# Kernel tuning notes

Measured on AMD Instinct MI355X. Metric: run time of the kernel, lower is better.

The kernel has to match this reference:

```python
import jax, jax.numpy as jnp
import numpy as np

B, NT, NZ, CIN, H, DOUT, L = 16, 128, 256, 3, 64, 128, 3
N = NT * NZ  # 32768 nodes
EPS = 1e-5


def _build_edges():
    # Toroidal grid: each node connects to 4 neighbors (wrap-around in theta and zeta).
    T, Z = np.meshgrid(np.arange(NT), np.arange(NZ), indexing='ij')
    curr = (T * NZ + Z).ravel()
    nbrs = np.stack([
        (((T + 1) % NT) * NZ + Z).ravel(),
        (((T - 1) % NT) * NZ + Z).ravel(),
        (T * NZ + (Z + 1) % NZ).ravel(),
        (T * NZ + (Z - 1) % NZ).ravel(),
    ], axis=1)
    src = np.repeat(curr, 4)
    dst = nbrs.ravel()
    return np.stack([src, dst]).astype(np.int32)  # (2, 4N)


def setup_inputs() -> dict:
    key = jax.random.key(0)
    ks = jax.random.split(key, 8)
    s = lambda k, shp, fan: jax.random.normal(k, shp, jnp.float32) / np.float32(np.sqrt(fan))
    return {
        'x': jax.random.normal(ks[0], (B, CIN, N), jnp.float32),
        'edge_index': jnp.asarray(_build_edges()),
        'embed_W': s(ks[1], (CIN, H), CIN),
        'embed_b': jnp.zeros((H,), jnp.float32),
        'mp_W1': s(ks[2], (L, 2 * H, H), 2 * H),
        'mp_b1': jnp.zeros((L, H), jnp.float32),
        'mp_g1': jnp.ones((L, H), jnp.float32),
        'mp_be1': jnp.zeros((L, H), jnp.float32),
        'mp_W2': s(ks[3], (L, H, H), H),
        'mp_b2': jnp.zeros((L, H), jnp.float32),
        'mp_g2': jnp.ones((L, H), jnp.float32),
        'mp_be2': jnp.zeros((L, H), jnp.float32),
        'head_W1': s(ks[4], (H, H), H),
        'head_b1': jnp.zeros((H,), jnp.float32),
        'head_W2': s(ks[5], (H, DOUT), H),
        'head_b2': jnp.zeros((DOUT,), jnp.float32),
    }


def _bn(y, g, b):
    # BatchNorm1d in training mode: biased batch stats over (batch*nodes).
    m = y.mean(axis=(0, 1))
    v = y.var(axis=(0, 1))
    return (y - m) * (g * jax.lax.rsqrt(v + EPS)) + b


def reference(x, edge_index, embed_W, embed_b, mp_W1, mp_b1, mp_g1, mp_be1,
              mp_W2, mp_b2, mp_g2, mp_be2, head_W1, head_b1, head_W2, head_b2):
    src, dst = edge_index[0], edge_index[1]
    # embedding: (B,3,N) -> (B,N,H)
    h = jax.nn.relu(jnp.einsum('bcn,ch->bnh', x, embed_W) + embed_b)
    deg = jnp.zeros((N,), x.dtype).at[dst].add(1.0)
    deg = jnp.clip(deg, 1.0)[None, :, None]  # (1,N,1), all 4 on this graph
    for l in range(L):
        # gather neighbor features and scatter-add to destination, mean aggregate
        agg = jnp.zeros_like(h).at[:, dst, :].add(h[:, src, :]) / deg
        comb = jnp.concatenate([h, agg], axis=-1)  # (B,N,2H)
        y = jax.nn.relu(_bn(comb @ mp_W1[l] + mp_b1[l], mp_g1[l], mp_be1[l]))
        y = jax.nn.relu(_bn(y @ mp_W2[l] + mp_b2[l], mp_g2[l], mp_be2[l]))
        h = y + h  # residual (c_in == c_out)
    pooled = h.mean(axis=1)  # AdaptiveAvgPool1d(1) over nodes
    return jax.nn.relu(pooled @ head_W1 + head_b1) @ head_W2 + head_b2
```

## Files before the change

kernel.cpp:

```cpp
#include <hip/hip_runtime.h>

typedef unsigned short u16;
typedef u16 u16x8 __attribute__((ext_vector_type(8)));
typedef short s16x8 __attribute__((ext_vector_type(8)));
typedef float f32x4 __attribute__((ext_vector_type(4)));

#define NNODES 32768
#define EPSV 1e-5f
#define INV_ROWS (1.0f / 524288.0f)

__device__ __forceinline__ float bf2f(u16 u) {
  union { unsigned int i; float f; } v; v.i = ((unsigned int)u) << 16; return v.f;
}
__device__ __forceinline__ u16 f2bf(float f) {
  union { float f; unsigned int i; } v; v.f = f;
  unsigned int r = v.i + 0x7FFFu + ((v.i >> 16) & 1u);
  return (u16)(r >> 16);
}

__global__ __launch_bounds__(256) void k_prep(
    const float* __restrict__ W1, const float* __restrict__ W2,
    u16* __restrict__ w1t, u16* __restrict__ w2t) {
  int idx = blockIdx.x * 256 + threadIdx.x;
  if (idx < 24576) {
    int l = idx >> 13, rem = idx & 8191;
    int n = rem >> 7, k = rem & 127;
    float w = W1[l * 8192 + k * 64 + n];
    if (k >= 64) w *= 0.25f;
    w1t[idx] = f2bf(w);
  } else {
    int idx2 = idx - 24576;
    if (idx2 < 12288) {
      int l = idx2 >> 12, rem = idx2 & 4095;
      int n = rem >> 6, k = rem & 63;
      w2t[idx2] = f2bf(W2[l * 4096 + k * 64 + n]);
    }
  }
}

__global__ __launch_bounds__(256) void k_embed(
    const float* __restrict__ x, const float* __restrict__ eW,
    const float* __restrict__ eb, u16* __restrict__ h) {
  int tid = threadIdx.x;
  int chunk = tid & 7;
  int r = blockIdx.x * 32 + (tid >> 3);
  int b = r >> 15;
  int n = r & 32767;
  const float* xb = x + (size_t)b * 3 * NNODES + n;
  float x0 = xb[0], x1 = xb[NNODES], x2 = xb[2 * NNODES];
  int c0 = chunk * 8;
  u16x8 ov;
#pragma unroll
  for (int j = 0; j < 8; ++j) {
    float acc = eb[c0 + j] + x0 * eW[c0 + j] + x1 * eW[64 + c0 + j] + x2 * eW[128 + c0 + j];
    ov[j] = f2bf(fmaxf(acc, 0.f));
  }
  *reinterpret_cast<u16x8*>(&h[(size_t)r * 64 + c0]) = ov;
}

#define RSTR 72
__global__ __launch_bounds__(256) void k_gemm1(
    const u16* __restrict__ h, u16* __restrict__ ybuf,
    const u16* __restrict__ w1t, const float* __restrict__ b1,
    float* __restrict__ sums) {
  __shared__ __align__(16) u16 buf[2][194 * RSTR];
  __shared__ __align__(16) u16 t_s[4][16 * RSTR];
  __shared__ float stat_s[4][128];

  int tid = threadIdx.x;
  int wv = tid >> 6, ln = tid & 63, ln15 = ln & 15, quad = ln >> 4;
  int blk = blockIdx.x;
  int xcd = blk & 7;
  int j = blk >> 3;
  int b = j >> 4;
  int t = xcd * 16 + (j & 15);
  const u16* hb = h + (((size_t)b) << 15) * 64;
  int tp = (t + 1) & 127, tm = (t + 127) & 127;

  s16x8 bfT[4][2], bfB[4][2];
#pragma unroll
  for (int c = 0; c < 4; ++c)
#pragma unroll
    for (int kk = 0; kk < 2; ++kk) {
      bfT[c][kk] = *reinterpret_cast<const s16x8*>(
          &w1t[(c * 16 + ln15) * 128 + kk * 32 + quad * 8]);
      bfB[c][kk] = *reinterpret_cast<const s16x8*>(
          &w1t[(c * 16 + ln15) * 128 + 64 + kk * 32 + quad * 8]);
    }

  float bias_c[4];
#pragma unroll
  for (int c = 0; c < 4; ++c) bias_c[c] = b1[c * 16 + ln15];

  float ls[4] = {0.f, 0.f, 0.f, 0.f}, ls2[4] = {0.f, 0.f, 0.f, 0.f};
  u16* ts = &t_s[wv][0];
  int cA = quad * 8;

  u16x8 R[7];
  auto ld_regs = [&](int q) {
    int z0 = q * 64;
#pragma unroll
    for (int ii = 0; ii < 7; ++ii) {
      int i = tid + ii * 256;
      if (i < 1552) {
        int c = i & 7;
        int r, rt, z;
        if (i < 528)       { r = i >> 3;          rt = t;  z = (z0 + 255 + r) & 255; }
        else if (i < 1040) { r = (i - 528) >> 3;  rt = tp; z = z0 + r; }
        else               { r = (i - 1040) >> 3; rt = tm; z = z0 + r; }
        R[ii] = *reinterpret_cast<const u16x8*>(
            &hb[((size_t)(rt * 256 + z)) * 64 + c * 8]);
      }
    }
  };
  auto wr_lds = [&](int bi) {
    u16* B = &buf[bi][0];
#pragma unroll
    for (int ii = 0; ii < 7; ++ii) {
      int i = tid + ii * 256;
      if (i < 1552) {
        int c = i & 7;
        int off;
        if (i < 528)       off = (i >> 3) * RSTR;
        else if (i < 1040) off = (66 + ((i - 528) >> 3)) * RSTR;
        else               off = (130 + ((i - 1040) >> 3)) * RSTR;
        *reinterpret_cast<u16x8*>(&B[off + c * 8]) = R[ii];
      }
    }
  };
  auto compute = [&](int q, int bi) {
    const u16* S  = &buf[bi][0];
    const u16* Tp = &buf[bi][66 * RSTR];
    const u16* Tm = &buf[bi][130 * RSTR];
    int lr = wv * 16 + ln15;

    s16x8 s0  = *reinterpret_cast<const s16x8*>(&S[(lr + 1) * RSTR + cA]);
    s16x8 s1  = *reinterpret_cast<const s16x8*>(&S[(lr + 1) * RSTR + 32 + cA]);
    s16x8 n0a = *reinterpret_cast<const s16x8*>(&Tp[lr * RSTR + cA]);
    s16x8 n0b = *reinterpret_cast<const s16x8*>(&Tp[lr * RSTR + 32 + cA]);
    s16x8 n1a = *reinterpret_cast<const s16x8*>(&Tm[lr * RSTR + cA]);
    s16x8 n1b = *reinterpret_cast<const s16x8*>(&Tm[lr * RSTR + 32 + cA]);
    s16x8 n2a = *reinterpret_cast<const s16x8*>(&S[(lr + 2) * RSTR + cA]);
    s16x8 n2b = *reinterpret_cast<const s16x8*>(&S[(lr + 2) * RSTR + 32 + cA]);
    s16x8 n3a = *reinterpret_cast<const s16x8*>(&S[lr * RSTR + cA]);
    s16x8 n3b = *reinterpret_cast<const s16x8*>(&S[lr * RSTR + 32 + cA]);

    f32x4 acc[4];
#pragma unroll
    for (int c = 0; c < 4; ++c) acc[c] = (f32x4){0.f, 0.f, 0.f, 0.f};
#pragma unroll
    for (int c = 0; c < 4; ++c) {
      acc[c] = __builtin_amdgcn_mfma_f32_16x16x32_bf16(s0,  bfT[c][0], acc[c], 0, 0, 0);
      acc[c] = __builtin_amdgcn_mfma_f32_16x16x32_bf16(s1,  bfT[c][1], acc[c], 0, 0, 0);
      acc[c] = __builtin_amdgcn_mfma_f32_16x16x32_bf16(n0a, bfB[c][0], acc[c], 0, 0, 0);
      acc[c] = __builtin_amdgcn_mfma_f32_16x16x32_bf16(n0b, bfB[c][1], acc[c], 0, 0, 0);
      acc[c] = __builtin_amdgcn_mfma_f32_16x16x32_bf16(n1a, bfB[c][0], acc[c], 0, 0, 0);
      acc[c] = __builtin_amdgcn_mfma_f32_16x16x32_bf16(n1b, bfB[c][1], acc[c], 0, 0, 0);
      acc[c] = __builtin_amdgcn_mfma_f32_16x16x32_bf16(n2a, bfB[c][0], acc[c], 0, 0, 0);
      acc[c] = __builtin_amdgcn_mfma_f32_16x16x32_bf16(n2b, bfB[c][1], acc[c], 0, 0, 0);
      acc[c] = __builtin_amdgcn_mfma_f32_16x16x32_bf16(n3a, bfB[c][0], acc[c], 0, 0, 0);
      acc[c] = __builtin_amdgcn_mfma_f32_16x16x32_bf16(n3b, bfB[c][1], acc[c], 0, 0, 0);
    }

    __builtin_amdgcn_wave_barrier();
#pragma unroll
    for (int c = 0; c < 4; ++c)
#pragma unroll
      for (int rg = 0; rg < 4; ++rg) {
        float vy = acc[c][rg] + bias_c[c];
        ls[c] += vy;
        ls2[c] += vy * vy;
        ts[(quad * 4 + rg) * RSTR + c * 16 + ln15] = f2bf(vy);
      }
    __builtin_amdgcn_wave_barrier();
    size_t R0 = (((size_t)b) << 15) + (size_t)t * 256 + q * 64 + wv * 16;
    int lr2 = ln >> 2;
#pragma unroll
    for (int p = 0; p < 2; ++p) {
      int ck = (ln & 3) + p * 4;
      u16x8 v = *reinterpret_cast<const u16x8*>(&ts[lr2 * RSTR + ck * 8]);
      *reinterpret_cast<u16x8*>(&ybuf[(R0 + lr2) * 64 + ck * 8]) = v;
    }
    __builtin_amdgcn_wave_barrier();
  };

  ld_regs(0);
  wr_lds(0);
  __syncthreads();
#pragma unroll 1
  for (int q = 0; q < 4; ++q) {
    if (q < 3) ld_regs(q + 1);
    compute(q, q & 1);
    if (q < 3) {
      wr_lds((q + 1) & 1);
      __syncthreads();
    }
  }

#pragma unroll
  for (int c = 0; c < 4; ++c) {
    ls[c]  += __shfl_xor(ls[c], 16, 64);  ls[c]  += __shfl_xor(ls[c], 32, 64);
    ls2[c] += __shfl_xor(ls2[c], 16, 64); ls2[c] += __shfl_xor(ls2[c], 32, 64);
  }
  if (ln < 16) {
#pragma unroll
    for (int c = 0; c < 4; ++c) {
      stat_s[wv][c * 16 + ln] = ls[c];
      stat_s[wv][64 + c * 16 + ln] = ls2[c];
    }
  }
  __syncthreads();
  if (tid < 128) {
    float s = stat_s[0][tid] + stat_s[1][tid] + stat_s[2][tid] + stat_s[3][tid];
    atomicAdd(&sums[xcd * 128 + tid], s);
  }
}

__global__ __launch_bounds__(256) void k_gemm2(
    u16* __restrict__ ybuf, const u16* __restrict__ w2t,
    const float* __restrict__ b2, const float* __restrict__ sums1,
    const float* __restrict__ g1, const float* __restrict__ be1,
    float* __restrict__ sums2) {
  __shared__ __align__(16) u16 t_s[4][16 * RSTR];
  __shared__ float s1_s[64], sh1_s[64];
  __shared__ float stat_s[4][128];

  int tid = threadIdx.x;
  int wv = tid >> 6, ln = tid & 63, ln15 = ln & 15, quad = ln >> 4;

  if (tid < 64) {
    float s = 0.f, s2 = 0.f;
#pragma unroll
    for (int sl = 0; sl < 8; ++sl) { s += sums1[sl * 128 + tid]; s2 += sums1[sl * 128 + 64 + tid]; }
    float m = s * INV_ROWS;
    float v = s2 * INV_ROWS - m * m;
    float sc = g1[tid] * rsqrtf(v + EPSV);
    s1_s[tid] = sc;
    sh1_s[tid] = be1[tid] - m * sc;
  }

  s16x8 bf[4][2];
#pragma unroll
  for (int c = 0; c < 4; ++c)
#pragma unroll
    for (int kk = 0; kk < 2; ++kk)
      bf[c][kk] = *reinterpret_cast<const s16x8*>(
          &w2t[(c * 16 + ln15) * 64 + kk * 32 + quad * 8]);

  float bias_c[4];
#pragma unroll
  for (int c = 0; c < 4; ++c) bias_c[c] = b2[c * 16 + ln15];

  __syncthreads();

  float sA[2][8], shA[2][8];
#pragma unroll
  for (int kk = 0; kk < 2; ++kk)
#pragma unroll
    for (int j = 0; j < 8; ++j) {
      int ch = kk * 32 + quad * 8 + j;
      sA[kk][j] = s1_s[ch];
      shA[kk][j] = sh1_s[ch];
    }

  float ls[4] = {0.f, 0.f, 0.f, 0.f}, ls2[4] = {0.f, 0.f, 0.f, 0.f};
  u16* ts = &t_s[wv][0];

  auto ld2 = [&](int it, u16x8* Y) {
    size_t row = (size_t)blockIdx.x * 256 + it * 64 + wv * 16 + ln15;
    Y[0] = *reinterpret_cast<const u16x8*>(&ybuf[row * 64 + quad * 8]);
    Y[1] = *reinterpret_cast<const u16x8*>(&ybuf[row * 64 + 32 + quad * 8]);
  };

  auto consume2 = [&](int it, u16x8* Y) {
    s16x8 a0, a1;
#pragma unroll
    for (int j = 0; j < 8; ++j) {
      a0[j] = (short)f2bf(fmaxf(bf2f(Y[0][j]) * sA[0][j] + shA[0][j], 0.f));
      a1[j] = (short)f2bf(fmaxf(bf2f(Y[1][j]) * sA[1][j] + shA[1][j], 0.f));
    }
    f32x4 acc[4];
#pragma unroll
    for (int c = 0; c < 4; ++c) acc[c] = (f32x4){0.f, 0.f, 0.f, 0.f};
#pragma unroll
    for (int c = 0; c < 4; ++c) {
      acc[c] = __builtin_amdgcn_mfma_f32_16x16x32_bf16(a0, bf[c][0], acc[c], 0, 0, 0);
      acc[c] = __builtin_amdgcn_mfma_f32_16x16x32_bf16(a1, bf[c][1], acc[c], 0, 0, 0);
    }
    __builtin_amdgcn_wave_barrier();
#pragma unroll
    for (int c = 0; c < 4; ++c)
#pragma unroll
      for (int rg = 0; rg < 4; ++rg) {
        float vy = acc[c][rg] + bias_c[c];
        ls[c] += vy;
        ls2[c] += vy * vy;
        ts[(quad * 4 + rg) * RSTR + c * 16 + ln15] = f2bf(vy);
      }
    __builtin_amdgcn_wave_barrier();
    size_t r0 = (size_t)blockIdx.x * 256 + it * 64 + wv * 16;
    int lr = ln >> 2;
#pragma unroll
    for (int p = 0; p < 2; ++p) {
      int ck = (ln & 3) + p * 4;
      u16x8 v = *reinterpret_cast<const u16x8*>(&ts[lr * RSTR + ck * 8]);
      *reinterpret_cast<u16x8*>(&ybuf[(r0 + lr) * 64 + ck * 8]) = v;
    }
    __builtin_amdgcn_wave_barrier();
  };

  u16x8 YA[2], YB[2];
  ld2(0, YA);
#pragma unroll 1
  for (int it = 0; it < 4; it += 2) {
    ld2(it + 1, YB);
    consume2(it, YA);
    if (it + 2 < 4) ld2(it + 2, YA);
    consume2(it + 1, YB);
  }

#pragma unroll
  for (int c = 0; c < 4; ++c) {
    ls[c]  += __shfl_xor(ls[c], 16, 64);  ls[c]  += __shfl_xor(ls[c], 32, 64);
    ls2[c] += __shfl_xor(ls2[c], 16, 64); ls2[c] += __shfl_xor(ls2[c], 32, 64);
  }
  if (ln < 16) {
#pragma unroll
    for (int c = 0; c < 4; ++c) {
      stat_s[wv][c * 16 + ln] = ls[c];
      stat_s[wv][64 + c * 16 + ln] = ls2[c];
    }
  }
  __syncthreads();
  if (tid < 128) {
    float s = stat_s[0][tid] + stat_s[1][tid] + stat_s[2][tid] + stat_s[3][tid];
    atomicAdd(&sums2[(blockIdx.x & 7) * 128 + tid], s);
  }
}

__global__ __launch_bounds__(256) void k_resid(
    u16* __restrict__ h, const u16* __restrict__ zbuf,
    const float* __restrict__ sums2, const float* __restrict__ g2,
    const float* __restrict__ be2, float* __restrict__ pooled) {
  __shared__ float s2_s[64], sh2_s[64];
  __shared__ float red_s[32][68];
  int tid = threadIdx.x;
  if (tid < 64) {
    float s = 0.f, s2 = 0.f;
#pragma unroll
    for (int sl = 0; sl < 8; ++sl) { s += sums2[sl * 128 + tid]; s2 += sums2[sl * 128 + 64 + tid]; }
    float m = s * INV_ROWS;
    float v = s2 * INV_ROWS - m * m;
    float sc = g2[tid] * rsqrtf(v + EPSV);
    s2_s[tid] = sc;
    sh2_s[tid] = be2[tid] - m * sc;
  }
  __syncthreads();
  int ch0 = (tid & 7) * 8;
  float scl[8], shl[8];
#pragma unroll
  for (int j = 0; j < 8; ++j) { scl[j] = s2_s[ch0 + j]; shl[j] = sh2_s[ch0 + j]; }
  float p[8] = {0.f, 0.f, 0.f, 0.f, 0.f, 0.f, 0.f, 0.f};
  bool do_pool = (pooled != nullptr);
  size_t base0 = (size_t)blockIdx.x * 16384 + tid * 8;
#pragma unroll 1
  for (int it = 0; it < 8; it += 2) {
    size_t ba = base0 + it * 2048;
    size_t bb = ba + 2048;
    u16x8 zva = *reinterpret_cast<const u16x8*>(&zbuf[ba]);
    u16x8 hva = *reinterpret_cast<const u16x8*>(&h[ba]);
    u16x8 zvb = *reinterpret_cast<const u16x8*>(&zbuf[bb]);
    u16x8 hvb = *reinterpret_cast<const u16x8*>(&h[bb]);
    u16x8 ova, ovb;
#pragma unroll
    for (int j = 0; j < 8; ++j) {
      float a = fmaxf(bf2f(zva[j]) * scl[j] + shl[j], 0.f);
      ova[j] = f2bf(bf2f(hva[j]) + a);
      p[j] += bf2f(ova[j]);
    }
#pragma unroll
    for (int j = 0; j < 8; ++j) {
      float a = fmaxf(bf2f(zvb[j]) * scl[j] + shl[j], 0.f);
      ovb[j] = f2bf(bf2f(hvb[j]) + a);
      p[j] += bf2f(ovb[j]);
    }
    if (!do_pool) {
      *reinterpret_cast<u16x8*>(&h[ba]) = ova;
      *reinterpret_cast<u16x8*>(&h[bb]) = ovb;
    }
  }
  if (do_pool) {
    int g = tid >> 3;
#pragma unroll
    for (int j = 0; j < 8; ++j) red_s[g][ch0 + j] = p[j];
    __syncthreads();
    if (tid < 64) {
      float s = 0.f;
#pragma unroll
      for (int gg = 0; gg < 32; ++gg) s += red_s[gg][tid];
      atomicAdd(&pooled[(blockIdx.x >> 7) * 64 + tid], s);
    }
  }
}

__global__ __launch_bounds__(256) void k_head(
    const float* __restrict__ pooled, const float* __restrict__ hW1,
    const float* __restrict__ hb1, const float* __restrict__ hW2,
    const float* __restrict__ hb2, float* __restrict__ out) {
  __shared__ float p_s[16 * 64];
  __shared__ float t1_s[16 * 64];
  int tid = threadIdx.x;
#pragma unroll
  for (int j = 0; j < 4; ++j)
    p_s[tid + 256 * j] = pooled[tid + 256 * j] * (1.0f / 32768.0f);
  __syncthreads();
#pragma unroll
  for (int j = 0; j < 4; ++j) {
    int idx = tid + 256 * j;
    int bb = idx >> 6, o = idx & 63;
    float acc = hb1[o];
    for (int k = 0; k < 64; ++k) acc += p_s[bb * 64 + k] * hW1[k * 64 + o];
    t1_s[idx] = fmaxf(acc, 0.f);
  }
  __syncthreads();
#pragma unroll
  for (int j = 0; j < 8; ++j) {
    int idx = tid + 256 * j;
    int bb = idx >> 7, o = idx & 127;
    float acc = hb2[o];
    for (int k = 0; k < 64; ++k) acc += t1_s[bb * 64 + k] * hW2[k * 128 + o];
    out[idx] = acc;
  }
}

extern "C" void kernel_launch(void* const* d_in, const int* in_sizes, int n_in,
                              void* d_out, int out_size, void* d_ws, size_t ws_size,
                              hipStream_t stream) {
  const float* x   = (const float*)d_in[0];
  const float* eW  = (const float*)d_in[2];
  const float* eb  = (const float*)d_in[3];
  const float* W1  = (const float*)d_in[4];
  const float* b1  = (const float*)d_in[5];
  const float* g1  = (const float*)d_in[6];
  const float* be1 = (const float*)d_in[7];
  const float* W2  = (const float*)d_in[8];
  const float* b2  = (const float*)d_in[9];
  const float* g2  = (const float*)d_in[10];
  const float* be2 = (const float*)d_in[11];
  const float* hW1 = (const float*)d_in[12];
  const float* hb1 = (const float*)d_in[13];
  const float* hW2 = (const float*)d_in[14];
  const float* hb2 = (const float*)d_in[15];
  float* out = (float*)d_out;

  char* ws = (char*)d_ws;
  u16* h    = (u16*)ws;
  u16* ybuf = (u16*)(ws + 67108864);
  float* stats  = (float*)(ws + 134217728);
  float* pooled = stats + 6144;
  u16* w1t = (u16*)(ws + 134217728 + 7168 * 4);
  u16* w2t = w1t + 24576;

  hipMemsetAsync(stats, 0, (6144 + 1024) * sizeof(float), stream);

  k_prep<<<144, 256, 0, stream>>>(W1, W2, w1t, w2t);
  k_embed<<<16384, 256, 0, stream>>>(x, eW, eb, h);
  for (int l = 0; l < 3; ++l) {
    float* sum1 = stats + l * 2048;
    float* sum2 = stats + l * 2048 + 1024;
    k_gemm1<<<2048, 256, 0, stream>>>(h, ybuf, w1t + l * 8192, b1 + l * 64, sum1);
    k_gemm2<<<2048, 256, 0, stream>>>(ybuf, w2t + l * 4096, b2 + l * 64,
                                      sum1, g1 + l * 64, be1 + l * 64, sum2);
    k_resid<<<2048, 256, 0, stream>>>(h, ybuf, sum2, g2 + l * 64, be2 + l * 64,
                                      (l == 2) ? pooled : nullptr);
  }
  k_head<<<1, 256, 0, stream>>>(pooled, hW1, hb1, hW2, hb2, out);
}
```

Baseline: 414.0 us.

## Process two theta rows per gemm1 block with XOR-swizzled LDS and fuse prep into embed

Each gemm1 block now handles two adjacent theta rows, loading four halo rows (t-1, t0, t1, t+1) so the middle rows are shared and fewer neighbor rows are reloaded from global memory. The grid is halved and each wave computes two 16-row tiles. LDS padding is replaced by an XOR chunk swizzle to avoid bank conflicts with a denser layout, which grows LDS use per block. Weight conversion is folded into the embed kernel, removing one launch.

```diff
diff --git a/kernel.cpp b/kernel.cpp
--- a/kernel.cpp
+++ b/kernel.cpp
@@ -18,29 +18,11 @@
   return (u16)(r >> 16);
 }
 
-__global__ __launch_bounds__(256) void k_prep(
+__global__ __launch_bounds__(256) void k_embed(
+    const float* __restrict__ x, const float* __restrict__ eW,
+    const float* __restrict__ eb, u16* __restrict__ h,
     const float* __restrict__ W1, const float* __restrict__ W2,
     u16* __restrict__ w1t, u16* __restrict__ w2t) {
-  int idx = blockIdx.x * 256 + threadIdx.x;
-  if (idx < 24576) {
-    int l = idx >> 13, rem = idx & 8191;
-    int n = rem >> 7, k = rem & 127;
-    float w = W1[l * 8192 + k * 64 + n];
-    if (k >= 64) w *= 0.25f;
-    w1t[idx] = f2bf(w);
-  } else {
-    int idx2 = idx - 24576;
-    if (idx2 < 12288) {
-      int l = idx2 >> 12, rem = idx2 & 4095;
-      int n = rem >> 6, k = rem & 63;
-      w2t[idx2] = f2bf(W2[l * 4096 + k * 64 + n]);
-    }
-  }
-}
-
-__global__ __launch_bounds__(256) void k_embed(
-    const float* __restrict__ x, const float* __restrict__ eW,
-    const float* __restrict__ eb, u16* __restrict__ h) {
   int tid = threadIdx.x;
   int chunk = tid & 7;
   int r = blockIdx.x * 32 + (tid >> 3);
@@ -56,15 +38,28 @@
     ov[j] = f2bf(fmaxf(acc, 0.f));
   }
   *reinterpret_cast<u16x8*>(&h[(size_t)r * 64 + c0]) = ov;
-}
-
-#define RSTR 72
+
+  int pidx = blockIdx.x * 256 + tid;
+  if (pidx < 24576) {
+    int l = pidx >> 13, rem = pidx & 8191;
+    int nn = rem >> 7, k = rem & 127;
+    float w = W1[l * 8192 + k * 64 + nn];
+    if (k >= 64) w *= 0.25f;
+    w1t[pidx] = f2bf(w);
+  } else if (pidx < 36864) {
+    int idx2 = pidx - 24576;
+    int l = idx2 >> 12, rem = idx2 & 4095;
+    int nn = rem >> 6, k = rem & 63;
+    w2t[idx2] = f2bf(W2[l * 4096 + k * 64 + nn]);
+  }
+}
+
 __global__ __launch_bounds__(256) void k_gemm1(
     const u16* __restrict__ h, u16* __restrict__ ybuf,
     const u16* __restrict__ w1t, const float* __restrict__ b1,
     float* __restrict__ sums) {
-  __shared__ __align__(16) u16 buf[2][194 * RSTR];
-  __shared__ __align__(16) u16 t_s[4][16 * RSTR];
+  __shared__ __align__(16) u16 buf[2][4 * 66 * 64];
+  __shared__ __align__(16) u16 t_s[4][16 * 64];
   __shared__ float stat_s[4][128];
 
   int tid = threadIdx.x;
@@ -72,10 +67,12 @@
   int blk = blockIdx.x;
   int xcd = blk & 7;
   int j = blk >> 3;
-  int b = j >> 4;
-  int t = xcd * 16 + (j & 15);
+  int b = j >> 3;
+  int local = j & 7;
+  int t0 = xcd * 16 + local * 2;
+  int t1 = t0 + 1;
   const u16* hb = h + (((size_t)b) << 15) * 64;
-  int tp = (t + 1) & 127, tm = (t + 127) & 127;
+  int tm = (t0 + 127) & 127, tp3 = (t1 + 1) & 127;
 
   s16x8 bfT[4][2], bfB[4][2];
 #pragma unroll
@@ -93,21 +90,19 @@
   for (int c = 0; c < 4; ++c) bias_c[c] = b1[c * 16 + ln15];
 
   float ls[4] = {0.f, 0.f, 0.f, 0.f}, ls2[4] = {0.f, 0.f, 0.f, 0.f};
-  u16* ts = &t_s[wv][0];
-  int cA = quad * 8;
-
-  u16x8 R[7];
+
+  u16x8 R[9];
   auto ld_regs = [&](int q) {
     int z0 = q * 64;
 #pragma unroll
-    for (int ii = 0; ii < 7; ++ii) {
+    for (int ii = 0; ii < 9; ++ii) {
       int i = tid + ii * 256;
-      if (i < 1552) {
+      if (i < 2112) {
+        int g = (i >= 1056) ? ((i >= 1584) ? 3 : 2) : ((i >= 528) ? 1 : 0);
+        int rr = (i - g * 528) >> 3;
         int c = i & 7;
-        int r, rt, z;
-        if (i < 528)       { r = i >> 3;          rt = t;  z = (z0 + 255 + r) & 255; }
-        else if (i < 1040) { r = (i - 528) >> 3;  rt = tp; z = z0 + r; }
-        else               { r = (i - 1040) >> 3; rt = tm; z = z0 + r; }
+        int rt = (g == 0) ? tm : (g == 1) ? t0 : (g == 2) ? t1 : tp3;
+        int z = (z0 + 255 + rr) & 255;
         R[ii] = *reinterpret_cast<const u16x8*>(
             &hb[((size_t)(rt * 256 + z)) * 64 + c * 8]);
       }
@@ -116,72 +111,85 @@
   auto wr_lds = [&](int bi) {
     u16* B = &buf[bi][0];
 #pragma unroll
-    for (int ii = 0; ii < 7; ++ii) {
+    for (int ii = 0; ii < 9; ++ii) {
       int i = tid + ii * 256;
-      if (i < 1552) {
+      if (i < 2112) {
+        int g = (i >= 1056) ? ((i >= 1584) ? 3 : 2) : ((i >= 528) ? 1 : 0);
+        int rr = (i - g * 528) >> 3;
         int c = i & 7;
-        int off;
-        if (i < 528)       off = (i >> 3) * RSTR;
-        else if (i < 1040) off = (66 + ((i - 528) >> 3)) * RSTR;
-        else               off = (130 + ((i - 1040) >> 3)) * RSTR;
-        *reinterpret_cast<u16x8*>(&B[off + c * 8]) = R[ii];
+        *reinterpret_cast<u16x8*>(
+            &B[(g * 66 + rr) * 64 + ((c ^ (rr & 7)) << 3)]) = R[ii];
       }
     }
   };
+  auto lds_rd = [&](const u16* base, int row, int chunk) {
+    return *reinterpret_cast<const s16x8*>(
+        &base[row * 64 + ((chunk ^ (row & 7)) << 3)]);
+  };
   auto compute = [&](int q, int bi) {
-    const u16* S  = &buf[bi][0];
-    const u16* Tp = &buf[bi][66 * RSTR];
-    const u16* Tm = &buf[bi][130 * RSTR];
-    int lr = wv * 16 + ln15;
-
-    s16x8 s0  = *reinterpret_cast<const s16x8*>(&S[(lr + 1) * RSTR + cA]);
-    s16x8 s1  = *reinterpret_cast<const s16x8*>(&S[(lr + 1) * RSTR + 32 + cA]);
-    s16x8 n0a = *reinterpret_cast<const s16x8*>(&Tp[lr * RSTR + cA]);
-    s16x8 n0b = *reinterpret_cast<const s16x8*>(&Tp[lr * RSTR + 32 + cA]);
-    s16x8 n1a = *reinterpret_cast<const s16x8*>(&Tm[lr * RSTR + cA]);
-    s16x8 n1b = *reinterpret_cast<const s16x8*>(&Tm[lr * RSTR + 32 + cA]);
-    s16x8 n2a = *reinterpret_cast<const s16x8*>(&S[(lr + 2) * RSTR + cA]);
-    s16x8 n2b = *reinterpret_cast<const s16x8*>(&S[(lr + 2) * RSTR + 32 + cA]);
-    s16x8 n3a = *reinterpret_cast<const s16x8*>(&S[lr * RSTR + cA]);
-    s16x8 n3b = *reinterpret_cast<const s16x8*>(&S[lr * RSTR + 32 + cA]);
-
-    f32x4 acc[4];
-#pragma unroll
-    for (int c = 0; c < 4; ++c) acc[c] = (f32x4){0.f, 0.f, 0.f, 0.f};
-#pragma unroll
-    for (int c = 0; c < 4; ++c) {
-      acc[c] = __builtin_amdgcn_mfma_f32_16x16x32_bf16(s0,  bfT[c][0], acc[c], 0, 0, 0);
-      acc[c] = __builtin_amdgcn_mfma_f32_16x16x32_bf16(s1,  bfT[c][1], acc[c], 0, 0, 0);
-      acc[c] = __builtin_amdgcn_mfma_f32_16x16x32_bf16(n0a, bfB[c][0], acc[c], 0, 0, 0);
-      acc[c] = __builtin_amdgcn_mfma_f32_16x16x32_bf16(n0b, bfB[c][1], acc[c], 0, 0, 0);
-      acc[c] = __builtin_amdgcn_mfma_f32_16x16x32_bf16(n1a, bfB[c][0], acc[c], 0, 0, 0);
-      acc[c] = __builtin_amdgcn_mfma_f32_16x16x32_bf16(n1b, bfB[c][1], acc[c], 0, 0, 0);
-      acc[c] = __builtin_amdgcn_mfma_f32_16x16x32_bf16(n2a, bfB[c][0], acc[c], 0, 0, 0);
-      acc[c] = __builtin_amdgcn_mfma_f32_16x16x32_bf16(n2b, bfB[c][1], acc[c], 0, 0, 0);
-      acc[c] = __builtin_amdgcn_mfma_f32_16x16x32_bf16(n3a, bfB[c][0], acc[c], 0, 0, 0);
-      acc[c] = __builtin_amdgcn_mfma_f32_16x16x32_bf16(n3b, bfB[c][1], acc[c], 0, 0, 0);
-    }
-
-    __builtin_amdgcn_wave_barrier();
-#pragma unroll
-    for (int c = 0; c < 4; ++c)
-#pragma unroll
-      for (int rg = 0; rg < 4; ++rg) {
-        float vy = acc[c][rg] + bias_c[c];
-        ls[c] += vy;
-        ls2[c] += vy * vy;
-        ts[(quad * 4 + rg) * RSTR + c * 16 + ln15] = f2bf(vy);
+    int tsel = wv >> 1;
+    const u16* Sb = &buf[bi][(1 + tsel) * 66 * 64];
+    const u16* Mb = &buf[bi][tsel * 66 * 64];
+    const u16* Pb = &buf[bi][(2 + tsel) * 66 * 64];
+    u16* ts = &t_s[wv][0];
+    int z0 = q * 64;
+#pragma unroll
+    for (int st = 0; st < 2; ++st) {
+      int zoff = (wv & 1) * 32 + st * 16;
+      int lz = zoff + ln15;
+
+      s16x8 s0 = lds_rd(Sb, lz + 1, quad);
+      s16x8 s1 = lds_rd(Sb, lz + 1, 4 + quad);
+      s16x8 pa = lds_rd(Pb, lz + 1, quad);
+      s16x8 pb = lds_rd(Pb, lz + 1, 4 + quad);
+      s16x8 ma = lds_rd(Mb, lz + 1, quad);
+      s16x8 mb = lds_rd(Mb, lz + 1, 4 + quad);
+      s16x8 za = lds_rd(Sb, lz + 2, quad);
+      s16x8 zb = lds_rd(Sb, lz + 2, 4 + quad);
+      s16x8 wa = lds_rd(Sb, lz, quad);
+      s16x8 wb = lds_rd(Sb, lz, 4 + quad);
+
+      f32x4 acc[4];
+#pragma unroll
+      for (int c = 0; c < 4; ++c) acc[c] = (f32x4){0.f, 0.f, 0.f, 0.f};
+#pragma unroll
+      for (int c = 0; c < 4; ++c) {
+        acc[c] = __builtin_amdgcn_mfma_f32_16x16x32_bf16(s0, bfT[c][0], acc[c], 0, 0, 0);
+        acc[c] = __builtin_amdgcn_mfma_f32_16x16x32_bf16(s1, bfT[c][1], acc[c], 0, 0, 0);
+        acc[c] = __builtin_amdgcn_mfma_f32_16x16x32_bf16(pa, bfB[c][0], acc[c], 0, 0, 0);
+        acc[c] = __builtin_amdgcn_mfma_f32_16x16x32_bf16(pb, bfB[c][1], acc[c], 0, 0, 0);
+        acc[c] = __builtin_amdgcn_mfma_f32_16x16x32_bf16(ma, bfB[c][0], acc[c], 0, 0, 0);
+        acc[c] = __builtin_amdgcn_mfma_f32_16x16x32_bf16(mb, bfB[c][1], acc[c], 0, 0, 0);
+        acc[c] = __builtin_amdgcn_mfma_f32_16x16x32_bf16(za, bfB[c][0], acc[c], 0, 0, 0);
+        acc[c] = __builtin_amdgcn_mfma_f32_16x16x32_bf16(zb, bfB[c][1], acc[c], 0, 0, 0);
+        acc[c] = __builtin_amdgcn_mfma_f32_16x16x32_bf16(wa, bfB[c][0], acc[c], 0, 0, 0);
+        acc[c] = __builtin_amdgcn_mfma_f32_16x16x32_bf16(wb, bfB[c][1], acc[c], 0, 0, 0);
       }
-    __builtin_amdgcn_wave_barrier();
-    size_t R0 = (((size_t)b) << 15) + (size_t)t * 256 + q * 64 + wv * 16;
-    int lr2 = ln >> 2;
-#pragma unroll
-    for (int p = 0; p < 2; ++p) {
-      int ck = (ln & 3) + p * 4;
-      u16x8 v = *reinterpret_cast<const u16x8*>(&ts[lr2 * RSTR + ck * 8]);
-      *reinterpret_cast<u16x8*>(&ybuf[(R0 + lr2) * 64 + ck * 8]) = v;
-    }
-    __builtin_amdgcn_wave_barrier();
+
+      __builtin_amdgcn_wave_barrier();
+#pragma unroll
+      for (int c = 0; c < 4; ++c)
+#pragma unroll
+        for (int rg = 0; rg < 4; ++rg) {
+          float vy = acc[c][rg] + bias_c[c];
+          ls[c] += vy;
+          ls2[c] += vy * vy;
+          int row = quad * 4 + rg;
+          int col = c * 16 + ln15;
+          ts[row * 64 + ((((col >> 3) ^ (row & 7))) << 3) + (col & 7)] = f2bf(vy);
+        }
+      __builtin_amdgcn_wave_barrier();
+      size_t R0 = (((size_t)b) << 15) + (size_t)((t0 + tsel) * 256) + z0 + zoff;
+      int lr2 = ln >> 2;
+#pragma unroll
+      for (int p = 0; p < 2; ++p) {
+        int ck = (ln & 3) + p * 4;
+        u16x8 v = *reinterpret_cast<const u16x8*>(
+            &ts[lr2 * 64 + ((ck ^ (lr2 & 7)) << 3)]);
+        *reinterpret_cast<u16x8*>(&ybuf[(R0 + lr2) * 64 + ck * 8]) = v;
+      }
+      __builtin_amdgcn_wave_barrier();
+    }
   };
 
   ld_regs(0);
@@ -216,6 +224,7 @@
   }
 }
 
+#define RSTR 72
 __global__ __launch_bounds__(256) void k_gemm2(
     u16* __restrict__ ybuf, const u16* __restrict__ w2t,
     const float* __restrict__ b2, const float* __restrict__ sums1,
@@ -463,12 +472,11 @@
 
   hipMemsetAsync(stats, 0, (6144 + 1024) * sizeof(float), stream);
 
-  k_prep<<<144, 256, 0, stream>>>(W1, W2, w1t, w2t);
-  k_embed<<<16384, 256, 0, stream>>>(x, eW, eb, h);
+  k_embed<<<16384, 256, 0, stream>>>(x, eW, eb, h, W1, W2, w1t, w2t);
   for (int l = 0; l < 3; ++l) {
     float* sum1 = stats + l * 2048;
     float* sum2 = stats + l * 2048 + 1024;
-    k_gemm1<<<2048, 256, 0, stream>>>(h, ybuf, w1t + l * 8192, b1 + l * 64, sum1);
+    k_gemm1<<<1024, 256, 0, stream>>>(h, ybuf, w1t + l * 8192, b1 + l * 64, sum1);
     k_gemm2<<<2048, 256, 0, stream>>>(ybuf, w2t + l * 4096, b2 + l * 64,
                                       sum1, g1 + l * 64, be1 + l * 64, sum2);
     k_resid<<<2048, 256, 0, stream>>>(h, ybuf, sum2, g2 + l * 64, be2 + l * 64,
```

After: 416.4 us. About the same (+0.6%).

## Stage gemm1 tiles with async global-to-LDS loads using XOR-swizzled h layout

Applied to the files above, without the earlier changes.

Stores h in global memory with 16-byte chunks XOR-swizzled by row, so k_gemm1 can copy tiles straight into unpadded LDS using global_load_lds. This removes the register staging and the separate LDS write pass, and the swizzle avoids LDS bank conflicts without padding. k_resid is adjusted to read the unswizzled zbuf against the swizzled h layout. The weight-prep kernel is folded into k_embed to drop one launch. The risk is that the swizzle must be consistent in every kernel that reads h, and any mismatch gives wrong results.

```diff
diff --git a/kernel.cpp b/kernel.cpp
--- a/kernel.cpp
+++ b/kernel.cpp
@@ -18,29 +18,18 @@
   return (u16)(r >> 16);
 }
 
-__global__ __launch_bounds__(256) void k_prep(
+__device__ __forceinline__ void gl_lds16(const void* g, void* l) {
+  __builtin_amdgcn_global_load_lds(
+      (const __attribute__((address_space(1))) unsigned int*)g,
+      (__attribute__((address_space(3))) unsigned int*)l, 16, 0, 0);
+}
+
+
+__global__ __launch_bounds__(256) void k_embed(
+    const float* __restrict__ x, const float* __restrict__ eW,
+    const float* __restrict__ eb, u16* __restrict__ h,
     const float* __restrict__ W1, const float* __restrict__ W2,
     u16* __restrict__ w1t, u16* __restrict__ w2t) {
-  int idx = blockIdx.x * 256 + threadIdx.x;
-  if (idx < 24576) {
-    int l = idx >> 13, rem = idx & 8191;
-    int n = rem >> 7, k = rem & 127;
-    float w = W1[l * 8192 + k * 64 + n];
-    if (k >= 64) w *= 0.25f;
-    w1t[idx] = f2bf(w);
-  } else {
-    int idx2 = idx - 24576;
-    if (idx2 < 12288) {
-      int l = idx2 >> 12, rem = idx2 & 4095;
-      int n = rem >> 6, k = rem & 63;
-      w2t[idx2] = f2bf(W2[l * 4096 + k * 64 + n]);
-    }
-  }
-}
-
-__global__ __launch_bounds__(256) void k_embed(
-    const float* __restrict__ x, const float* __restrict__ eW,
-    const float* __restrict__ eb, u16* __restrict__ h) {
   int tid = threadIdx.x;
   int chunk = tid & 7;
   int r = blockIdx.x * 32 + (tid >> 3);
@@ -55,16 +44,30 @@
     float acc = eb[c0 + j] + x0 * eW[c0 + j] + x1 * eW[64 + c0 + j] + x2 * eW[128 + c0 + j];
     ov[j] = f2bf(fmaxf(acc, 0.f));
   }
-  *reinterpret_cast<u16x8*>(&h[(size_t)r * 64 + c0]) = ov;
-}
-
-#define RSTR 72
+  int phys = chunk ^ (r & 7);
+  *reinterpret_cast<u16x8*>(&h[(size_t)r * 64 + phys * 8]) = ov;
+
+  int pidx = blockIdx.x * 256 + tid;
+  if (pidx < 24576) {
+    int l = pidx >> 13, rem = pidx & 8191;
+    int nn = rem >> 7, k = rem & 127;
+    float w = W1[l * 8192 + k * 64 + nn];
+    if (k >= 64) w *= 0.25f;
+    w1t[pidx] = f2bf(w);
+  } else if (pidx < 36864) {
+    int idx2 = pidx - 24576;
+    int l = idx2 >> 12, rem = idx2 & 4095;
+    int nn = rem >> 6, k = rem & 63;
+    w2t[idx2] = f2bf(W2[l * 4096 + k * 64 + nn]);
+  }
+}
+
 __global__ __launch_bounds__(256) void k_gemm1(
     const u16* __restrict__ h, u16* __restrict__ ybuf,
     const u16* __restrict__ w1t, const float* __restrict__ b1,
     float* __restrict__ sums) {
-  __shared__ __align__(16) u16 buf[2][194 * RSTR];
-  __shared__ __align__(16) u16 t_s[4][16 * RSTR];
+  __shared__ __align__(16) u16 buf[2][194 * 64];
+  __shared__ __align__(16) u16 t_s[4][16 * 72];
   __shared__ float stat_s[4][128];
 
   int tid = threadIdx.x;
@@ -93,57 +96,42 @@
   for (int c = 0; c < 4; ++c) bias_c[c] = b1[c * 16 + ln15];
 
   float ls[4] = {0.f, 0.f, 0.f, 0.f}, ls2[4] = {0.f, 0.f, 0.f, 0.f};
-  u16* ts = &t_s[wv][0];
-  int cA = quad * 8;
-
-  u16x8 R[7];
-  auto ld_regs = [&](int q) {
+
+  auto stage_async = [&](int q, int bi) {
     int z0 = q * 64;
+    u16* B = &buf[bi][0];
 #pragma unroll
     for (int ii = 0; ii < 7; ++ii) {
       int i = tid + ii * 256;
       if (i < 1552) {
-        int c = i & 7;
-        int r, rt, z;
-        if (i < 528)       { r = i >> 3;          rt = t;  z = (z0 + 255 + r) & 255; }
-        else if (i < 1040) { r = (i - 528) >> 3;  rt = tp; z = z0 + r; }
-        else               { r = (i - 1040) >> 3; rt = tm; z = z0 + r; }
-        R[ii] = *reinterpret_cast<const u16x8*>(
-            &hb[((size_t)(rt * 256 + z)) * 64 + c * 8]);
+        int rr, rt, z;
+        if (i < 528)       { rr = i >> 3;          rt = t;  z = (z0 + 255 + rr) & 255; }
+        else if (i < 1040) { rr = (i - 528) >> 3;  rt = tp; z = z0 + rr; }
+        else               { rr = (i - 1040) >> 3; rt = tm; z = z0 + rr; }
+        gl_lds16(&hb[((size_t)(rt * 256 + z)) * 64 + (i & 7) * 8], &B[(size_t)i * 8]);
       }
     }
   };
-  auto wr_lds = [&](int bi) {
-    u16* B = &buf[bi][0];
-#pragma unroll
-    for (int ii = 0; ii < 7; ++ii) {
-      int i = tid + ii * 256;
-      if (i < 1552) {
-        int c = i & 7;
-        int off;
-        if (i < 528)       off = (i >> 3) * RSTR;
-        else if (i < 1040) off = (66 + ((i - 528) >> 3)) * RSTR;
-        else               off = (130 + ((i - 1040) >> 3)) * RSTR;
-        *reinterpret_cast<u16x8*>(&B[off + c * 8]) = R[ii];
-      }
-    }
+  auto lds_rd = [&](const u16* base, int row, int chunk, int key) {
+    return *reinterpret_cast<const s16x8*>(
+        &base[row * 64 + ((chunk ^ (key & 7)) << 3)]);
   };
   auto compute = [&](int q, int bi) {
     const u16* S  = &buf[bi][0];
-    const u16* Tp = &buf[bi][66 * RSTR];
-    const u16* Tm = &buf[bi][130 * RSTR];
+    const u16* Tp = &buf[bi][66 * 64];
+    const u16* Tm = &buf[bi][130 * 64];
+    u16* ts = &t_s[wv][0];
     int lr = wv * 16 + ln15;
-
-    s16x8 s0  = *reinterpret_cast<const s16x8*>(&S[(lr + 1) * RSTR + cA]);
-    s16x8 s1  = *reinterpret_cast<const s16x8*>(&S[(lr + 1) * RSTR + 32 + cA]);
-    s16x8 n0a = *reinterpret_cast<const s16x8*>(&Tp[lr * RSTR + cA]);
-    s16x8 n0b = *reinterpret_cast<const s16x8*>(&Tp[lr * RSTR + 32 + cA]);
-    s16x8 n1a = *reinterpret_cast<const s16x8*>(&Tm[lr * RSTR + cA]);
-    s16x8 n1b = *reinterpret_cast<const s16x8*>(&Tm[lr * RSTR + 32 + cA]);
-    s16x8 n2a = *reinterpret_cast<const s16x8*>(&S[(lr + 2) * RSTR + cA]);
-    s16x8 n2b = *reinterpret_cast<const s16x8*>(&S[(lr + 2) * RSTR + 32 + cA]);
-    s16x8 n3a = *reinterpret_cast<const s16x8*>(&S[lr * RSTR + cA]);
-    s16x8 n3b = *reinterpret_cast<const s16x8*>(&S[lr * RSTR + 32 + cA]);
+    s16x8 s0  = lds_rd(S, lr + 1, quad, lr);
+    s16x8 s1  = lds_rd(S, lr + 1, 4 + quad, lr);
+    s16x8 n0a = lds_rd(Tp, lr, quad, lr);
+    s16x8 n0b = lds_rd(Tp, lr, 4 + quad, lr);
+    s16x8 n1a = lds_rd(Tm, lr, quad, lr);
+    s16x8 n1b = lds_rd(Tm, lr, 4 + quad, lr);
+    s16x8 n2a = lds_rd(S, lr + 2, quad, lr + 1);
+    s16x8 n2b = lds_rd(S, lr + 2, 4 + quad, lr + 1);
+    s16x8 n3a = lds_rd(S, lr, quad, lr + 7);
+    s16x8 n3b = lds_rd(S, lr, 4 + quad, lr + 7);
 
     f32x4 acc[4];
 #pragma unroll
@@ -170,7 +158,7 @@
         float vy = acc[c][rg] + bias_c[c];
         ls[c] += vy;
         ls2[c] += vy * vy;
-        ts[(quad * 4 + rg) * RSTR + c * 16 + ln15] = f2bf(vy);
+        ts[(quad * 4 + rg) * 72 + c * 16 + ln15] = f2bf(vy);
       }
     __builtin_amdgcn_wave_barrier();
     size_t R0 = (((size_t)b) << 15) + (size_t)t * 256 + q * 64 + wv * 16;
@@ -178,23 +166,19 @@
 #pragma unroll
     for (int p = 0; p < 2; ++p) {
       int ck = (ln & 3) + p * 4;
-      u16x8 v = *reinterpret_cast<const u16x8*>(&ts[lr2 * RSTR + ck * 8]);
+      u16x8 v = *reinterpret_cast<const u16x8*>(&ts[lr2 * 72 + ck * 8]);
       *reinterpret_cast<u16x8*>(&ybuf[(R0 + lr2) * 64 + ck * 8]) = v;
     }
     __builtin_amdgcn_wave_barrier();
   };
 
-  ld_regs(0);
-  wr_lds(0);
+  stage_async(0, 0);
   __syncthreads();
 #pragma unroll 1
   for (int q = 0; q < 4; ++q) {
-    if (q < 3) ld_regs(q + 1);
+    if (q < 3) stage_async(q + 1, (q + 1) & 1);
     compute(q, q & 1);
-    if (q < 3) {
-      wr_lds((q + 1) & 1);
-      __syncthreads();
-    }
+    if (q < 3) __syncthreads();
   }
 
 #pragma unroll
@@ -216,6 +200,7 @@
   }
 }
 
+#define RSTR 72
 __global__ __launch_bounds__(256) void k_gemm2(
     u16* __restrict__ ybuf, const u16* __restrict__ w2t,
     const float* __restrict__ b2, const float* __restrict__ sums1,
@@ -356,33 +341,37 @@
     sh2_s[tid] = be2[tid] - m * sc;
   }
   __syncthreads();
-  int ch0 = (tid & 7) * 8;
+  int p = tid & 7;
+  int key = (tid >> 3) & 7;
+  int c = p ^ key;
+  int ch0 = c * 8;
   float scl[8], shl[8];
 #pragma unroll
   for (int j = 0; j < 8; ++j) { scl[j] = s2_s[ch0 + j]; shl[j] = sh2_s[ch0 + j]; }
-  float p[8] = {0.f, 0.f, 0.f, 0.f, 0.f, 0.f, 0.f, 0.f};
+  float pacc[8] = {0.f, 0.f, 0.f, 0.f, 0.f, 0.f, 0.f, 0.f};
   bool do_pool = (pooled != nullptr);
   size_t base0 = (size_t)blockIdx.x * 16384 + tid * 8;
+  ptrdiff_t zoff = (ptrdiff_t)(c - p) * 8;
 #pragma unroll 1
   for (int it = 0; it < 8; it += 2) {
     size_t ba = base0 + it * 2048;
     size_t bb = ba + 2048;
-    u16x8 zva = *reinterpret_cast<const u16x8*>(&zbuf[ba]);
+    u16x8 zva = *reinterpret_cast<const u16x8*>(&zbuf[ba + zoff]);
     u16x8 hva = *reinterpret_cast<const u16x8*>(&h[ba]);
-    u16x8 zvb = *reinterpret_cast<const u16x8*>(&zbuf[bb]);
+    u16x8 zvb = *reinterpret_cast<const u16x8*>(&zbuf[bb + zoff]);
     u16x8 hvb = *reinterpret_cast<const u16x8*>(&h[bb]);
     u16x8 ova, ovb;
 #pragma unroll
     for (int j = 0; j < 8; ++j) {
       float a = fmaxf(bf2f(zva[j]) * scl[j] + shl[j], 0.f);
       ova[j] = f2bf(bf2f(hva[j]) + a);
-      p[j] += bf2f(ova[j]);
+      pacc[j] += bf2f(ova[j]);
     }
 #pragma unroll
     for (int j = 0; j < 8; ++j) {
       float a = fmaxf(bf2f(zvb[j]) * scl[j] + shl[j], 0.f);
       ovb[j] = f2bf(bf2f(hvb[j]) + a);
-      p[j] += bf2f(ovb[j]);
+      pacc[j] += bf2f(ovb[j]);
     }
     if (!do_pool) {
       *reinterpret_cast<u16x8*>(&h[ba]) = ova;
@@ -392,7 +381,7 @@
   if (do_pool) {
     int g = tid >> 3;
 #pragma unroll
-    for (int j = 0; j < 8; ++j) red_s[g][ch0 + j] = p[j];
+    for (int j = 0; j < 8; ++j) red_s[g][ch0 + j] = pacc[j];
     __syncthreads();
     if (tid < 64) {
       float s = 0.f;
@@ -463,8 +452,7 @@
 
   hipMemsetAsync(stats, 0, (6144 + 1024) * sizeof(float), stream);
 
-  k_prep<<<144, 256, 0, stream>>>(W1, W2, w1t, w2t);
-  k_embed<<<16384, 256, 0, stream>>>(x, eW, eb, h);
+  k_embed<<<16384, 256, 0, stream>>>(x, eW, eb, h, W1, W2, w1t, w2t);
   for (int l = 0; l < 3; ++l) {
     float* sum1 = stats + l * 2048;
     float* sum2 = stats + l * 2048 + 1024;
```

Result: no change. 413.5 us (-0.1%).
